# Kernel tuning notes

Measured on AMD Instinct MI355X. Metric: run time of the kernel, lower is better.

Reference implementation:

```python
import jax, jax.numpy as jnp
import numpy as np

N_NODES = 128   # num_nodes
BATCH = 4096
HIDDEN = 32     # fixed by the module's Linear(N+1, 32)


def setup_inputs() -> dict:
    key = jax.random.key(0)
    ks = jax.random.split(key, 8)
    N, B, H = N_NODES, BATCH, HIDDEN
    x = jax.random.normal(ks[0], (B, N), dtype=jnp.float32)
    # adjacency masks: A[b, :, j] = parent indicator of node j in sample b
    A = (jax.random.uniform(ks[1], (B, N, N)) < 0.3).astype(jnp.float32)
    # per-sample topological permutation
    order = jax.vmap(lambda k: jax.random.permutation(k, N))(
        jax.random.split(ks[2], B)).astype(jnp.int32)
    # intervention target per sample, -1 = no intervention
    do_idxs = jax.random.randint(ks[3], (B,), -1, N, dtype=jnp.int32)
    # externalized intervention noise (torch.normal in the original forward)
    u = jax.random.normal(ks[4], (B,), dtype=jnp.float32)
    # stacked per-node MLP params: Linear(N+1, 32) -> LeakyReLU -> Linear(32, 1)
    W1 = jax.random.normal(ks[5], (N, N + 1, H), dtype=jnp.float32) / np.sqrt(N + 1)
    b1 = jnp.zeros((N, H), dtype=jnp.float32)
    W2 = jax.random.normal(ks[6], (N, H, 1), dtype=jnp.float32) / np.sqrt(H)
    b2 = jnp.zeros((N, 1), dtype=jnp.float32)
    return dict(x=x, A=A, u=u, W1=W1, b1=b1, W2=W2, b2=b2,
                order=order, do_idxs=do_idxs)


def reference(x, A, u, W1, b1, W2, b2, order, do_idxs):
    B, N = x.shape
    bidx = jnp.arange(B)
    # set intervened entries: outputs[b, do_idxs[b]] = u[b] where do_idxs != -1
    outputs0 = jnp.where(do_idxs[:, None] == jnp.arange(N)[None, :],
                         u[:, None], jnp.zeros_like(x))

    def step(outputs, node):           # node: [B] current node per sample
        mask = A[bidx, :, node]        # [B, N] parent mask of this node
        ins = jnp.concatenate([mask * outputs,
                               x[bidx, node][:, None]], axis=1)  # [B, N+1]
        # per-node MLP gathered by node id (grouped tiny GEMMs)
        h = jax.nn.leaky_relu(jnp.einsum('bd,bdh->bh', ins, W1[node]) + b1[node])
        out = (jnp.einsum('bh,bho->bo', h, W2[node]) + b2[node])[:, 0]  # [B]
        # intervened samples keep their value u (they are skipped in the original)
        new_val = jnp.where(do_idxs == node, outputs[bidx, node], out)
        return outputs.at[bidx, node].set(new_val), None

    outputs, _ = jax.lax.scan(step, outputs0, order.T)  # sequential topo order
    return outputs
```

## Files before the change

kernel.cpp:

```cpp
#include <hip/hip_runtime.h>
#include <stdint.h>

#define NN 128
#define BB 4096
#define HH 32

typedef float f4 __attribute__((ext_vector_type(4)));

__global__ __launch_bounds__(256) void pack_bits(const float* __restrict__ A,
                                                 ulonglong2* __restrict__ bitsT) {
    const int tid = blockIdx.x * 256 + threadIdx.x;
    const int b   = tid >> 5;
    const int ng  = (tid & 31) << 2;
    const float* Ab = A + (size_t)b * (NN * NN) + ng;
    unsigned long long w0[4] = {0ull, 0ull, 0ull, 0ull};
    unsigned long long w1[4] = {0ull, 0ull, 0ull, 0ull};
#pragma unroll 8
    for (int d = 0; d < 64; ++d) {
        f4 v = __builtin_nontemporal_load((const f4*)(Ab + (size_t)d * NN));
        const unsigned long long bit = 1ull << d;
        if (v[0] != 0.f) w0[0] |= bit;
        if (v[1] != 0.f) w0[1] |= bit;
        if (v[2] != 0.f) w0[2] |= bit;
        if (v[3] != 0.f) w0[3] |= bit;
    }
#pragma unroll 8
    for (int d = 0; d < 64; ++d) {
        f4 v = __builtin_nontemporal_load((const f4*)(Ab + (size_t)(d + 64) * NN));
        const unsigned long long bit = 1ull << d;
        if (v[0] != 0.f) w1[0] |= bit;
        if (v[1] != 0.f) w1[1] |= bit;
        if (v[2] != 0.f) w1[2] |= bit;
        if (v[3] != 0.f) w1[3] |= bit;
    }
    ulonglong2* o = bitsT + b * NN + ng;
#pragma unroll
    for (int i = 0; i < 4; ++i) {
        ulonglong2 r; r.x = w0[i]; r.y = w1[i];
        o[i] = r;
    }
}

__device__ __forceinline__ int mbcnt64(unsigned long long m) {
    return __builtin_amdgcn_mbcnt_hi((unsigned int)(m >> 32),
           __builtin_amdgcn_mbcnt_lo((unsigned int)m, 0));
}
__device__ __forceinline__ unsigned long long rfl64(unsigned long long v) {
    unsigned int lo = __builtin_amdgcn_readfirstlane((unsigned int)v);
    unsigned int hi = __builtin_amdgcn_readfirstlane((unsigned int)(v >> 32));
    return ((unsigned long long)hi << 32) | lo;
}

#define STEP(T, ECUR, ENXT, BCUR, BNXT)                                      \
  {                                                                          \
    const char* WnB = (const char*)(W1 + (size_t)node0 * ((NN + 1) * HH));   \
                \
    float wv[16];                                                            \
    _Pragma("unroll")                                                        \
    for (int q = 0; q < 8; ++q) {                                            \
        wv[2*q]   = *(const float*)(WnB + (__float_as_int(ECUR[q][1]) + j4));\
        wv[2*q+1] = *(const float*)(WnB + (__float_as_int(ECUR[q][3]) + j4));\
    }                                                                        \
                                  \
    if ((T) > 0) {                                                           \
        if (dob != pend_node && lane == (pend_node & 63)) {                  \
            if (pend_node < 64) out0 = pend_val; else out1 = pend_val;       \
        }                                                                    \
        if (pend_node < 64) nz0 |= 1ull << pend_node;                        \
        else                nz1 |= 1ull << (pend_node - 64);                 \
    }                                                                        \
      \
    const unsigned long long bw0n = rfl64(vbn.x);                            \
    const unsigned long long bw1n = rfl64(vbn.y);                            \
    const unsigned long long m0 = nz0 & bw0n;                                \
    const unsigned long long m1 = nz1 & bw1n;                                \
    const int c0n  = __popcll(m0);                                           \
    const int cntn = c0n + __popcll(m1);                                     \
            \
    {                                                                        \
        const int p0 = mbcnt64(m0);                                          \
        if (m0 & lanebit)                                                    \
            entb[BNXT][p0 & 1][p0 >> 1] = make_float2(out0, fidx0);          \
        const int p1 = c0n + mbcnt64(m1);                                    \
        if (m1 & lanebit)                                                    \
            entb[BNXT][p1 & 1][p1 >> 1] = make_float2(out1, fidx1);          \
        const int top = (cntn > 32) ? 48 : 32;                               \
        const int pp = cntn + lane;                                          \
        if (pp < top)                                                        \
            entb[BNXT][pp & 1][pp >> 1] = make_float2(0.f, __int_as_float(0));\
    }                                                                        \
    \
    {                                                                        \
        const f4* eb = (const f4*)&entb[BNXT][half][0];                      \
        _Pragma("unroll")                                                    \
        for (int q = 0; q < 8; ++q) ENXT[q] = eb[q];                         \
    }                                                                        \
                     \
    const int node2 = ((T) + 2 < NN)                                         \
        ? __builtin_amdgcn_readfirstlane(ord[(T) + 2]) : 0;                  \
    const ulonglong2 vb2 = bb[node2];                                        \
    const float* Wn_nxt = W1 + (size_t)node1 * ((NN + 1) * HH);              \
    const float w2v_n  = W2[node1 * HH + j];                                 \
    const float b1v_n  = b1[node1 * HH + j];                                 \
    const float xv_n   = x[b * NN + node1];                                  \
    const float b2v_n  = b2[node1];                                          \
    const float w1xv_n = Wn_nxt[NN * HH + j];                                \
    const float wfr_n  = Wn_nxt[(node0 << 5) + j];                           \
                         \
    float a0 = 0.f, a1 = 0.f, a2 = 0.f, a3 = 0.f;                            \
    _Pragma("unroll")                                                        \
    for (int q = 0; q < 8; q += 2) {                                         \
        a0 += ECUR[q][0]     * wv[2*q];                                      \
        a1 += ECUR[q][2]     * wv[2*q+1];                                    \
        a2 += ECUR[q+1][0]   * wv[2*q+2];                                    \
        a3 += ECUR[q+1][2]   * wv[2*q+3];                                    \
    }                                                                        \
    \
    if (cnt_c > 32) {                                                        \
        f4 e3[4];                                                            \
        const f4* eb3 = (const f4*)&entb[BCUR][half][16];                    \
        _Pragma("unroll")                                                    \
        for (int q = 0; q < 4; ++q) e3[q] = eb3[q];                          \
        float w3[8];                                                         \
        _Pragma("unroll")                                                    \
        for (int q = 0; q < 4; ++q) {                                        \
            w3[2*q]   = *(const float*)(WnB + (__float_as_int(e3[q][1]) + j4));\
            w3[2*q+1] = *(const float*)(WnB + (__float_as_int(e3[q][3]) + j4));\
        }                                                                    \
        _Pragma("unroll")                                                    \
        for (int q = 0; q < 4; ++q) {                                        \
            a0 += e3[q][0] * w3[2*q];                                        \
            a1 += e3[q][2] * w3[2*q+1];                                      \
        }                                                                    \
             \
        if (cnt_c > 48) {                                                    \
            for (int i = 24; 2 * i + half < cnt_c; ++i) {                    \
                float2 e = entb[BCUR][half][i];                              \
                a2 += e.x * *(const float*)(WnB + (__float_as_int(e.y) + j4));\
            }                                                                \
        }                                                                    \
    }                                                                        \
    float acc = (a0 + a1) + (a2 + a3);                                       \
                                                       \
    float accT = acc + __shfl_xor(acc, 32);                                  \
    const bool fc = ((T) > 0) && (dob != pend_node) &&                       \
        ((((pend_node < 64) ? (bw0c >> pend_node)                            \
                            : (bw1c >> (pend_node - 64)))) & 1ull);          \
    accT += (fc ? pend_val : 0.f) * wfr;                                     \
    accT += xv * w1xv;                                                       \
    accT += b1v;                                                             \
    const float hv = (accT > 0.f) ? accT : 0.01f * accT;                     \
    float pr = hv * w2v;                                                     \
    pr += __int_as_float(__builtin_amdgcn_update_dpp(                        \
             0, __float_as_int(pr), 0xB1, 0xF, 0xF, true));                  \
    pr += __int_as_float(__builtin_amdgcn_update_dpp(                        \
             0, __float_as_int(pr), 0x4E, 0xF, 0xF, true));                  \
    pr += __int_as_float(__builtin_amdgcn_update_dpp(                        \
             0, __float_as_int(pr), 0x141, 0xF, 0xF, true));                 \
    pr += __int_as_float(__builtin_amdgcn_update_dpp(                        \
             0, __float_as_int(pr), 0x140, 0xF, 0xF, true));                 \
    pr += __shfl_xor(pr, 16);                                                \
    const float outv = pr + b2v;                                             \
    pend_node = node0; pend_val = outv;                                      \
                                                              \
    node0 = node1; node1 = node2;                                            \
    bw0c = bw0n; bw1c = bw1n; vbn = vb2;                                     \
    w2v = w2v_n; b1v = b1v_n; xv = xv_n; b2v = b2v_n;                        \
    w1xv = w1xv_n; wfr = wfr_n;                                              \
    cnt_c = cntn;                                                            \
  }

__global__ __launch_bounds__(64, 4) void cond_mlp(
    const float* __restrict__ x, const float* __restrict__ u,
    const float* __restrict__ W1, const float* __restrict__ b1,
    const float* __restrict__ W2, const float* __restrict__ b2,
    const int* __restrict__ order, const int* __restrict__ do_idxs,
    const ulonglong2* __restrict__ bitsT, float* __restrict__ out)
{
    const int b = blockIdx.x;
    const int lane = threadIdx.x;
    const int j = lane & 31;
    const int j4 = j << 2;
    const int half = lane >> 5;

    __shared__ __align__(16) float2 entb[2][2][68];

    const float ub = u[b];
    const int dob = __builtin_amdgcn_readfirstlane(do_idxs[b]);
    float out0 = (dob == lane) ? ub : 0.f;
    float out1 = (dob == lane + 64) ? ub : 0.f;

    unsigned long long nz0 = (dob >= 0 && dob < 64) ? (1ull << dob) : 0ull;
    unsigned long long nz1 = (dob >= 64) ? (1ull << (dob - 64)) : 0ull;

    const int* ord = order + b * NN;
    const ulonglong2* bb = bitsT + (size_t)b * NN;

    const unsigned long long lanebit = 1ull << lane;
    const float fidx0 = __int_as_float(lane << 7);
    const float fidx1 = __int_as_float((lane + 64) << 7);

    int node0 = __builtin_amdgcn_readfirstlane(ord[0]);
    int node1 = __builtin_amdgcn_readfirstlane(ord[1]);
    const ulonglong2 vb0 = bb[node0];
    ulonglong2 vbn = bb[node1];

    unsigned long long bw0c = rfl64(vb0.x);
    unsigned long long bw1c = rfl64(vb0.y);
    int cnt_c;
    f4 eA[8], eB[8];
    {
        const unsigned long long m0 = nz0 & bw0c;
        const unsigned long long m1 = nz1 & bw1c;
        const int c0 = __popcll(m0);
        cnt_c = c0 + __popcll(m1);
        const int p0 = mbcnt64(m0);
        if (m0 & lanebit) entb[0][p0 & 1][p0 >> 1] = make_float2(out0, fidx0);
        const int p1 = c0 + mbcnt64(m1);
        if (m1 & lanebit) entb[0][p1 & 1][p1 >> 1] = make_float2(out1, fidx1);
        const int top = (cnt_c > 32) ? 48 : 32;
        const int pp = cnt_c + lane;
        if (pp < top) entb[0][pp & 1][pp >> 1] = make_float2(0.f, __int_as_float(0));
        const f4* eb = (const f4*)&entb[0][half][0];
#pragma unroll
        for (int q = 0; q < 8; ++q) eA[q] = eb[q];
    }

    const float* Wn0 = W1 + (size_t)node0 * ((NN + 1) * HH);
    float w2v  = W2[node0 * HH + j];
    float b1v  = b1[node0 * HH + j];
    float xv   = x[b * NN + node0];
    float b2v  = b2[node0];
    float w1xv = Wn0[NN * HH + j];
    float wfr  = 0.f;

    int pend_node = 0;
    float pend_val = 0.f;

    for (int t = 0; t < NN; t += 2) {
        STEP(t,     eA, eB, 0, 1)
        STEP(t + 1, eB, eA, 1, 0)
    }

    if (dob != pend_node && lane == (pend_node & 63)) {
        if (pend_node < 64) out0 = pend_val; else out1 = pend_val;
    }

    out[b * NN + lane] = out0;
    out[b * NN + 64 + lane] = out1;
}

extern "C" void kernel_launch(void* const* d_in, const int* in_sizes, int n_in,
                              void* d_out, int out_size, void* d_ws, size_t ws_size,
                              hipStream_t stream) {
    const float* x   = (const float*)d_in[0];
    const float* A   = (const float*)d_in[1];
    const float* u   = (const float*)d_in[2];
    const float* W1  = (const float*)d_in[3];
    const float* b1  = (const float*)d_in[4];
    const float* W2  = (const float*)d_in[5];
    const float* b2  = (const float*)d_in[6];
    const int* order = (const int*)d_in[7];
    const int* dox   = (const int*)d_in[8];

    ulonglong2* bitsT = (ulonglong2*)d_ws;

    pack_bits<<<(BB * 32) / 256, 256, 0, stream>>>(A, bitsT);
    cond_mlp<<<BB, 64, 0, stream>>>(x, u, W1, b1, W2, b2, order, dox,
                                    bitsT, (float*)d_out);
}
```

Before: 527.1 us.

## Split bit packing across four threads per column and ping-pong pipeline state

```diff
diff --git a/kernel.cpp b/kernel.cpp
--- a/kernel.cpp
+++ b/kernel.cpp
@@ -10,35 +10,23 @@
 __global__ __launch_bounds__(256) void pack_bits(const float* __restrict__ A,
                                                  ulonglong2* __restrict__ bitsT) {
     const int tid = blockIdx.x * 256 + threadIdx.x;
-    const int b   = tid >> 5;
-    const int ng  = (tid & 31) << 2;
-    const float* Ab = A + (size_t)b * (NN * NN) + ng;
-    unsigned long long w0[4] = {0ull, 0ull, 0ull, 0ull};
-    unsigned long long w1[4] = {0ull, 0ull, 0ull, 0ull};
+    const int b  = tid >> 7;
+    const int q  = (tid >> 5) & 3;
+    const int ng = (tid & 31) << 2;
+    const float* Ab = A + (size_t)b * (NN * NN) + (size_t)(q * 32) * NN + ng;
+    unsigned int w[4] = {0u, 0u, 0u, 0u};
 #pragma unroll 8
-    for (int d = 0; d < 64; ++d) {
+    for (int d = 0; d < 32; ++d) {
         f4 v = __builtin_nontemporal_load((const f4*)(Ab + (size_t)d * NN));
-        const unsigned long long bit = 1ull << d;
-        if (v[0] != 0.f) w0[0] |= bit;
-        if (v[1] != 0.f) w0[1] |= bit;
-        if (v[2] != 0.f) w0[2] |= bit;
-        if (v[3] != 0.f) w0[3] |= bit;
-    }
-#pragma unroll 8
-    for (int d = 0; d < 64; ++d) {
-        f4 v = __builtin_nontemporal_load((const f4*)(Ab + (size_t)(d + 64) * NN));
-        const unsigned long long bit = 1ull << d;
-        if (v[0] != 0.f) w1[0] |= bit;
-        if (v[1] != 0.f) w1[1] |= bit;
-        if (v[2] != 0.f) w1[2] |= bit;
-        if (v[3] != 0.f) w1[3] |= bit;
-    }
-    ulonglong2* o = bitsT + b * NN + ng;
+        const unsigned int bit = 1u << d;
+        if (v[0] != 0.f) w[0] |= bit;
+        if (v[1] != 0.f) w[1] |= bit;
+        if (v[2] != 0.f) w[2] |= bit;
+        if (v[3] != 0.f) w[3] |= bit;
+    }
+    unsigned int* o = (unsigned int*)(bitsT + (size_t)b * NN + ng);
 #pragma unroll
-    for (int i = 0; i < 4; ++i) {
-        ulonglong2 r; r.x = w0[i]; r.y = w1[i];
-        o[i] = r;
-    }
+    for (int i = 0; i < 4; ++i) o[i * 4 + q] = w[i];
 }
 
 __device__ __forceinline__ int mbcnt64(unsigned long long m) {
@@ -51,17 +39,26 @@
     return ((unsigned long long)hi << 32) | lo;
 }
 
-#define STEP(T, ECUR, ENXT, BCUR, BNXT)                                      \
+struct Pipe {
+    int node;
+    int cnt;
+    unsigned long long bw0, bw1;
+    ulonglong2 vb;
+    float w2v, b1v, xv, b2v, w1xv, wfr;
+};
+
+#define STEP(T, ECUR, ENXT, SC, SN, BCUR, BNXT)                              \
   {                                                                          \
-    const char* WnB = (const char*)(W1 + (size_t)node0 * ((NN + 1) * HH));   \
-                \
+    const int nodeT = SC.node;                                               \
+    const char* WnB = (const char*)(W1 + (size_t)nodeT * ((NN + 1) * HH));   \
+                                                                      \
     float wv[16];                                                            \
     _Pragma("unroll")                                                        \
     for (int q = 0; q < 8; ++q) {                                            \
         wv[2*q]   = *(const float*)(WnB + (__float_as_int(ECUR[q][1]) + j4));\
         wv[2*q+1] = *(const float*)(WnB + (__float_as_int(ECUR[q][3]) + j4));\
     }                                                                        \
-                                  \
+                                                                      \
     if ((T) > 0) {                                                           \
         if (dob != pend_node && lane == (pend_node & 63)) {                  \
             if (pend_node < 64) out0 = pend_val; else out1 = pend_val;       \
@@ -69,14 +66,15 @@
         if (pend_node < 64) nz0 |= 1ull << pend_node;                        \
         else                nz1 |= 1ull << (pend_node - 64);                 \
     }                                                                        \
-      \
-    const unsigned long long bw0n = rfl64(vbn.x);                            \
-    const unsigned long long bw1n = rfl64(vbn.y);                            \
+                                                                      \
+    const unsigned long long bw0n = rfl64(SN.vb.x);                          \
+    const unsigned long long bw1n = rfl64(SN.vb.y);                          \
     const unsigned long long m0 = nz0 & bw0n;                                \
     const unsigned long long m1 = nz1 & bw1n;                                \
     const int c0n  = __popcll(m0);                                           \
     const int cntn = c0n + __popcll(m1);                                     \
-            \
+    SN.bw0 = bw0n; SN.bw1 = bw1n; SN.cnt = cntn;                             \
+                                                                      \
     {                                                                        \
         const int p0 = mbcnt64(m0);                                          \
         if (m0 & lanebit)                                                    \
@@ -89,24 +87,27 @@
         if (pp < top)                                                        \
             entb[BNXT][pp & 1][pp >> 1] = make_float2(0.f, __int_as_float(0));\
     }                                                                        \
-    \
+                                                                      \
     {                                                                        \
         const f4* eb = (const f4*)&entb[BNXT][half][0];                      \
         _Pragma("unroll")                                                    \
         for (int q = 0; q < 8; ++q) ENXT[q] = eb[q];                         \
     }                                                                        \
-                     \
+                                                                      \
     const int node2 = ((T) + 2 < NN)                                         \
         ? __builtin_amdgcn_readfirstlane(ord[(T) + 2]) : 0;                  \
-    const ulonglong2 vb2 = bb[node2];                                        \
-    const float* Wn_nxt = W1 + (size_t)node1 * ((NN + 1) * HH);              \
-    const float w2v_n  = W2[node1 * HH + j];                                 \
-    const float b1v_n  = b1[node1 * HH + j];                                 \
-    const float xv_n   = x[b * NN + node1];                                  \
-    const float b2v_n  = b2[node1];                                          \
-    const float w1xv_n = Wn_nxt[NN * HH + j];                                \
-    const float wfr_n  = Wn_nxt[(node0 << 5) + j];                           \
-                         \
+    SC.node = node2;                                                         \
+    SC.vb   = bb[node2];                                                     \
+    {                                                                        \
+        const float* Wn_nxt = W1 + (size_t)SN.node * ((NN + 1) * HH);        \
+        SN.w2v  = W2[SN.node * HH + j];                                      \
+        SN.b1v  = b1[SN.node * HH + j];                                      \
+        SN.xv   = x[b * NN + SN.node];                                       \
+        SN.b2v  = b2[SN.node];                                               \
+        SN.w1xv = Wn_nxt[NN * HH + j];                                       \
+        SN.wfr  = Wn_nxt[(nodeT << 5) + j];                                  \
+    }                                                                        \
+                                                                      \
     float a0 = 0.f, a1 = 0.f, a2 = 0.f, a3 = 0.f;                            \
     _Pragma("unroll")                                                        \
     for (int q = 0; q < 8; q += 2) {                                         \
@@ -115,8 +116,8 @@
         a2 += ECUR[q+1][0]   * wv[2*q+2];                                    \
         a3 += ECUR[q+1][2]   * wv[2*q+3];                                    \
     }                                                                        \
-    \
-    if (cnt_c > 32) {                                                        \
+                 \
+    if (SC_cnt_snap > 32) {                                                  \
         f4 e3[4];                                                            \
         const f4* eb3 = (const f4*)&entb[BCUR][half][16];                    \
         _Pragma("unroll")                                                    \
@@ -133,24 +134,24 @@
             a1 += e3[q][2] * w3[2*q+1];                                      \
         }                                                                    \
              \
-        if (cnt_c > 48) {                                                    \
-            for (int i = 24; 2 * i + half < cnt_c; ++i) {                    \
+        if (SC_cnt_snap > 48) {                                              \
+            for (int i = 24; 2 * i + half < SC_cnt_snap; ++i) {              \
                 float2 e = entb[BCUR][half][i];                              \
                 a2 += e.x * *(const float*)(WnB + (__float_as_int(e.y) + j4));\
             }                                                                \
         }                                                                    \
     }                                                                        \
     float acc = (a0 + a1) + (a2 + a3);                                       \
-                                                       \
+                                                                      \
     float accT = acc + __shfl_xor(acc, 32);                                  \
     const bool fc = ((T) > 0) && (dob != pend_node) &&                       \
-        ((((pend_node < 64) ? (bw0c >> pend_node)                            \
-                            : (bw1c >> (pend_node - 64)))) & 1ull);          \
-    accT += (fc ? pend_val : 0.f) * wfr;                                     \
-    accT += xv * w1xv;                                                       \
-    accT += b1v;                                                             \
+        ((((pend_node < 64) ? (SC.bw0 >> pend_node)                          \
+                            : (SC.bw1 >> (pend_node - 64)))) & 1ull);        \
+    accT += (fc ? pend_val : 0.f) * SC.wfr;                                  \
+    accT += SC.xv * SC.w1xv;                                                 \
+    accT += SC.b1v;                                                          \
     const float hv = (accT > 0.f) ? accT : 0.01f * accT;                     \
-    float pr = hv * w2v;                                                     \
+    float pr = hv * SC.w2v;                                                  \
     pr += __int_as_float(__builtin_amdgcn_update_dpp(                        \
              0, __float_as_int(pr), 0xB1, 0xF, 0xF, true));                  \
     pr += __int_as_float(__builtin_amdgcn_update_dpp(                        \
@@ -160,14 +161,8 @@
     pr += __int_as_float(__builtin_amdgcn_update_dpp(                        \
              0, __float_as_int(pr), 0x140, 0xF, 0xF, true));                 \
     pr += __shfl_xor(pr, 16);                                                \
-    const float outv = pr + b2v;                                             \
-    pend_node = node0; pend_val = outv;                                      \
-                                                              \
-    node0 = node1; node1 = node2;                                            \
-    bw0c = bw0n; bw1c = bw1n; vbn = vb2;                                     \
-    w2v = w2v_n; b1v = b1v_n; xv = xv_n; b2v = b2v_n;                        \
-    w1xv = w1xv_n; wfr = wfr_n;                                              \
-    cnt_c = cntn;                                                            \
+    const float outv = pr + SC.b2v;                                          \
+    pend_node = nodeT; pend_val = outv;                                      \
   }
 
 __global__ __launch_bounds__(64, 4) void cond_mlp(
@@ -200,46 +195,51 @@
     const float fidx0 = __int_as_float(lane << 7);
     const float fidx1 = __int_as_float((lane + 64) << 7);
 
-    int node0 = __builtin_amdgcn_readfirstlane(ord[0]);
-    int node1 = __builtin_amdgcn_readfirstlane(ord[1]);
-    const ulonglong2 vb0 = bb[node0];
-    ulonglong2 vbn = bb[node1];
-
-    unsigned long long bw0c = rfl64(vb0.x);
-    unsigned long long bw1c = rfl64(vb0.y);
-    int cnt_c;
+    Pipe SA, SB;
+    SA.node = __builtin_amdgcn_readfirstlane(ord[0]);
+    SB.node = __builtin_amdgcn_readfirstlane(ord[1]);
+    SB.vb = bb[SB.node];
+    SA.vb = bb[SA.node];
+
+    SA.bw0 = rfl64(SA.vb.x);
+    SA.bw1 = rfl64(SA.vb.y);
     f4 eA[8], eB[8];
     {
-        const unsigned long long m0 = nz0 & bw0c;
-        const unsigned long long m1 = nz1 & bw1c;
+        const unsigned long long m0 = nz0 & SA.bw0;
+        const unsigned long long m1 = nz1 & SA.bw1;
         const int c0 = __popcll(m0);
-        cnt_c = c0 + __popcll(m1);
+        SA.cnt = c0 + __popcll(m1);
         const int p0 = mbcnt64(m0);
         if (m0 & lanebit) entb[0][p0 & 1][p0 >> 1] = make_float2(out0, fidx0);
         const int p1 = c0 + mbcnt64(m1);
         if (m1 & lanebit) entb[0][p1 & 1][p1 >> 1] = make_float2(out1, fidx1);
-        const int top = (cnt_c > 32) ? 48 : 32;
-        const int pp = cnt_c + lane;
+        const int top = (SA.cnt > 32) ? 48 : 32;
+        const int pp = SA.cnt + lane;
         if (pp < top) entb[0][pp & 1][pp >> 1] = make_float2(0.f, __int_as_float(0));
         const f4* eb = (const f4*)&entb[0][half][0];
 #pragma unroll
         for (int q = 0; q < 8; ++q) eA[q] = eb[q];
     }
-
-    const float* Wn0 = W1 + (size_t)node0 * ((NN + 1) * HH);
-    float w2v  = W2[node0 * HH + j];
-    float b1v  = b1[node0 * HH + j];
-    float xv   = x[b * NN + node0];
-    float b2v  = b2[node0];
-    float w1xv = Wn0[NN * HH + j];
-    float wfr  = 0.f;
+    {
+        const float* Wn0 = W1 + (size_t)SA.node * ((NN + 1) * HH);
+        SA.w2v  = W2[SA.node * HH + j];
+        SA.b1v  = b1[SA.node * HH + j];
+        SA.xv   = x[b * NN + SA.node];
+        SA.b2v  = b2[SA.node];
+        SA.w1xv = Wn0[NN * HH + j];
+        SA.wfr  = 0.f;
+    }
 
     int pend_node = 0;
     float pend_val = 0.f;
 
     for (int t = 0; t < NN; t += 2) {
-        STEP(t,     eA, eB, 0, 1)
-        STEP(t + 1, eB, eA, 1, 0)
+        const int SC_cnt_snap0 = SA.cnt;
+        { const int SC_cnt_snap = SC_cnt_snap0;
+          STEP(t,     eA, eB, SA, SB, 0, 1) }
+        const int SC_cnt_snap1 = SB.cnt;
+        { const int SC_cnt_snap = SC_cnt_snap1;
+          STEP(t + 1, eB, eA, SB, SA, 1, 0) }
     }
 
     if (dob != pend_node && lane == (pend_node & 63)) {
@@ -265,7 +265,7 @@
 
     ulonglong2* bitsT = (ulonglong2*)d_ws;
 
-    pack_bits<<<(BB * 32) / 256, 256, 0, stream>>>(A, bitsT);
+    pack_bits<<<(BB * 128) / 256, 256, 0, stream>>>(A, bitsT);
     cond_mlp<<<BB, 64, 0, stream>>>(x, u, W1, b1, W2, b2, order, dox,
                                     bitsT, (float*)d_out);
 }
```

New measurement: 516.6 us. 2.0% less time.
